# Kernel tuning notes

Hardware: AMD Instinct MI355X
Metric: run time of the kernel (lower is better)

## Reference

```python
import jax, jax.numpy as jnp
import numpy as np

BATCH = 65536
VEC = 512       # CLIP embedding dim
K = 1024        # num_cluster
GAMMA = 0.99
EPS = 1e-05


def setup_inputs() -> dict:
    key = jax.random.key(0)
    k1, k2, k3 = jax.random.split(key, 3)
    batch_vectors = jax.random.normal(k1, (BATCH, VEC), dtype=jnp.float32)
    weight = jax.random.normal(k2, (VEC, K), dtype=jnp.float32)        # codebook, stored (vec_size, num_cluster)
    cluster_size = jnp.ones((K,), dtype=jnp.float32)
    embed_avg = jax.random.normal(k3, (VEC, K), dtype=jnp.float32)
    return {
        "batch_vectors": batch_vectors,
        "weight": weight,
        "cluster_size": cluster_size,
        "embed_avg": embed_avg,
    }


def reference(batch_vectors, weight, cluster_size, embed_avg):
    """One minibatch_update step of clusteringEMA_torch.

    Returns the updated codebook `weight` of shape (vec_size, num_cluster).
    """
    gamma = GAMMA
    eps = EPS
    num_cluster = weight.shape[1]

    # nearest centroid: squared L2 distance has the same argmin as the L2 norm
    x2 = jnp.sum(batch_vectors * batch_vectors, axis=1, keepdims=True)   # (B,1)
    w2 = jnp.sum(weight * weight, axis=0)[None, :]                       # (1,K)
    dist2 = x2 + w2 - 2.0 * (batch_vectors @ weight)                     # (B,K)
    argmin = jnp.argmin(dist2, axis=-1)                                  # (B,)

    # per-cluster counts (one-hot sum), zeros replaced by 1
    counts = jnp.zeros((num_cluster,), dtype=batch_vectors.dtype).at[argmin].add(1.0)
    n_idx_choice = jnp.where(counts == 0, 1.0, counts)

    # EMA of cluster sizes
    new_cluster_size = gamma * cluster_size + (1.0 - gamma) * n_idx_choice

    # embed_sum = x^T @ onehot  == per-cluster sum of assigned vectors, (vec,K)
    embed_sum = jax.ops.segment_sum(batch_vectors, argmin, num_segments=num_cluster).T
    new_embed_avg = gamma * embed_avg + (1.0 - gamma) * embed_sum

    # Laplace-smoothed normalization
    n = jnp.sum(new_cluster_size)
    cs = (new_cluster_size + eps) / (n + num_cluster * eps) * n
    new_weight = new_embed_avg / cs[None, :]
    return new_weight
```

## Files before the change

### kernel.cpp

```cpp
#include <hip/hip_runtime.h>

typedef unsigned int uint;
typedef unsigned short ushort_t;
typedef unsigned long long u64;
typedef __attribute__((ext_vector_type(4))) float f32x4;
typedef __attribute__((ext_vector_type(8))) __bf16 bf16x8;
typedef __attribute__((ext_vector_type(8))) unsigned short us8;

#define BATCH 65536
#define VEC 512
#define K 1024
#define GAMMA 0.99f
#define EPS 1e-05f
#define SEG 64
#define MARGIN 0.75f

#define NKT (VEC / 64)
#define TG 2048

__device__ __forceinline__ ushort_t rtn(float f) {
    uint u = __float_as_uint(f);
    return (ushort_t)((u + 0x7FFFu + ((u >> 16) & 1u)) >> 16);
}

__device__ __forceinline__ void gl16(const void* g, void* l) {
    __builtin_amdgcn_global_load_lds(
        (const __attribute__((address_space(1))) unsigned int*)g,
        (__attribute__((address_space(3))) unsigned int*)l, 16, 0, 0);
}

__device__ __forceinline__ float dec_key(uint e) {
    uint b = (e & 0x80000000u) ? (e & 0x7FFFFFFFu) : ~e;
    return __uint_as_float(b);
}

#define BC8(p) __builtin_bit_cast(bf16x8, (p))

__global__ void k_pack_w(const float* __restrict__ w, us8* __restrict__ wpk,
                         float* __restrict__ wT, float* __restrict__ w2p,
                         int* __restrict__ cc ) {
    __shared__ float lds[32][257];
    const int g = blockIdx.x;
    const int gx = g >> 3, kt = g & 7;
    const int t = threadIdx.x;

    float s = 0.f;
#pragma unroll
    for (int ih = 0; ih < 2; ++ih) {
        __syncthreads();
#pragma unroll
        for (int r = 0; r < 32; ++r)
            lds[r][t] = w[(size_t)(kt * 64 + ih * 32 + r) * K + gx * 256 + t];
        __syncthreads();

#pragma unroll
        for (int r = 0; r < 32; ++r) { float f = lds[r][t]; s += f * f; }

#pragma unroll
        for (int i = 0; i < 4; ++i) {
            const int c = i * 256 + t;
            const int ct = c >> 6, lane = c & 63;
            const int cl = ct * 16 + (lane & 15);
            const int r0 = (lane >> 4) * 8;
            us8 v;
#pragma unroll
            for (int j = 0; j < 8; ++j) v[j] = rtn(lds[r0 + j][cl]);
            wpk[(size_t)g * TG + ct * 128 + ih * 64 + lane] = v;
        }

#pragma unroll
        for (int rr = 0; rr < 8; ++rr) {
            f32x4 v = {lds[rr * 4 + 0][t], lds[rr * 4 + 1][t],
                       lds[rr * 4 + 2][t], lds[rr * 4 + 3][t]};
            *(f32x4*)&wT[(size_t)(gx * 256 + t) * VEC + kt * 64 + ih * 32 + rr * 4] = v;
        }
    }
    w2p[kt * K + gx * 256 + t] = s;

    if (g < 8) cc[g * 256 + t] = 0;
    if (g == 8 && t == 0) cc[2048] = 0;
}

__global__ void k_pack_x(const float* __restrict__ x, us8* __restrict__ xpk) {
    const int blk = blockIdx.x;
    const int gy = blk >> 3, kt = blk & 7;
    const int t = threadIdx.x;
#pragma unroll
    for (int i = 0; i < 8; ++i) {
        const int g = i * 256 + t;
        const int slab = g >> 7, ksub = (g >> 6) & 1, lane = g & 63;
        const int row = gy * 256 + slab * 16 + (lane & 15);
        const int k = kt * 64 + ksub * 32 + ((lane >> 4) << 3);
        const f32x4 q0 = *(const f32x4*)&x[(size_t)row * VEC + k];
        const f32x4 q1 = *(const f32x4*)&x[(size_t)row * VEC + k + 4];
        us8 v;
#pragma unroll
        for (int j = 0; j < 4; ++j) { v[j] = rtn(q0[j]); v[4 + j] = rtn(q1[j]); }
        xpk[(size_t)blk * TG + g] = v;
    }
}

__launch_bounds__(512, 2)
__global__ void k_gemm(const us8* __restrict__ xpk, const us8* __restrict__ wpk,
                       const float* __restrict__ w2p,
                       u64* __restrict__ keysA, u64* __restrict__ keysB) {
    __shared__ us8 lds[2][2 * TG];

    const int blk = blockIdx.x;
    const int ord = blk >> 3;
    const int gy = (blk & 7) * 32 + (ord >> 2);
    const int gx = ord & 3;
    const int t = threadIdx.x;
    const int lane = t & 63;
    const int wv = t >> 6;
    const int wm = wv >> 2;
    const int wn = wv & 3;

    const us8* asrc = xpk + (size_t)gy * (NKT * TG);
    const us8* bsrc = wpk + (size_t)gx * (NKT * TG);

    auto stage = [&](int slot, int kt) {
        const us8* sa = asrc + (size_t)kt * TG;
        const us8* sb = bsrc + (size_t)kt * TG;
#pragma unroll
        for (int i = 0; i < 4; ++i) gl16(sa + i * 512 + t, &lds[slot][i * 512 + t]);
#pragma unroll
        for (int i = 0; i < 4; ++i) gl16(sb + i * 512 + t, &lds[slot][TG + i * 512 + t]);
    };

    f32x4 acc[8][4];
#pragma unroll
    for (int i = 0; i < 8; ++i)
#pragma unroll
        for (int j = 0; j < 4; ++j) acc[i][j] = (f32x4){0.f, 0.f, 0.f, 0.f};

    stage(0, 0);
    stage(1, 1);

    for (int kt = 0; kt < NKT; ++kt) {
        const int buf = kt & 1;
        if (kt >= 1 && kt + 1 < NKT) {
            stage(buf ^ 1, kt + 1);
            asm volatile("s_waitcnt vmcnt(8)" ::: "memory");
        } else if (kt == 0) {
            asm volatile("s_waitcnt vmcnt(8)" ::: "memory");
        } else {
            asm volatile("s_waitcnt vmcnt(0)" ::: "memory");
        }
        __builtin_amdgcn_s_barrier();

        const us8* A = &lds[buf][0];
        const us8* B = &lds[buf][TG];
        bf16x8 ah[8], b0, b1;

#pragma unroll
        for (int rt = 0; rt < 8; ++rt) ah[rt] = BC8(A[(wm * 8 + rt) * 128 + lane]);
        b0 = BC8(B[(wn * 4 + 0) * 128 + lane]);
        b1 = BC8(B[(wn * 4 + 1) * 128 + lane]);
        __builtin_amdgcn_s_barrier();
        asm volatile("s_waitcnt lgkmcnt(0)" ::: "memory");
        __builtin_amdgcn_sched_barrier(0);
        __builtin_amdgcn_s_setprio(1);
#pragma unroll
        for (int rt = 0; rt < 8; ++rt) {
            acc[rt][0] = __builtin_amdgcn_mfma_f32_16x16x32_bf16(ah[rt], b0, acc[rt][0], 0, 0, 0);
            acc[rt][1] = __builtin_amdgcn_mfma_f32_16x16x32_bf16(ah[rt], b1, acc[rt][1], 0, 0, 0);
        }
        __builtin_amdgcn_s_setprio(0);
        __builtin_amdgcn_s_barrier();

        b0 = BC8(B[(wn * 4 + 2) * 128 + lane]);
        b1 = BC8(B[(wn * 4 + 3) * 128 + lane]);
        __builtin_amdgcn_s_barrier();
        asm volatile("s_waitcnt lgkmcnt(0)" ::: "memory");
        __builtin_amdgcn_sched_barrier(0);
        __builtin_amdgcn_s_setprio(1);
#pragma unroll
        for (int rt = 0; rt < 8; ++rt) {
            acc[rt][2] = __builtin_amdgcn_mfma_f32_16x16x32_bf16(ah[rt], b0, acc[rt][2], 0, 0, 0);
            acc[rt][3] = __builtin_amdgcn_mfma_f32_16x16x32_bf16(ah[rt], b1, acc[rt][3], 0, 0, 0);
        }
        __builtin_amdgcn_s_setprio(0);
        __builtin_amdgcn_s_barrier();

#pragma unroll
        for (int rt = 0; rt < 8; ++rt) ah[rt] = BC8(A[(wm * 8 + rt) * 128 + 64 + lane]);
        b0 = BC8(B[(wn * 4 + 0) * 128 + 64 + lane]);
        b1 = BC8(B[(wn * 4 + 1) * 128 + 64 + lane]);
        __builtin_amdgcn_s_barrier();
        asm volatile("s_waitcnt lgkmcnt(0)" ::: "memory");
        __builtin_amdgcn_sched_barrier(0);
        __builtin_amdgcn_s_setprio(1);
#pragma unroll
        for (int rt = 0; rt < 8; ++rt) {
            acc[rt][0] = __builtin_amdgcn_mfma_f32_16x16x32_bf16(ah[rt], b0, acc[rt][0], 0, 0, 0);
            acc[rt][1] = __builtin_amdgcn_mfma_f32_16x16x32_bf16(ah[rt], b1, acc[rt][1], 0, 0, 0);
        }
        __builtin_amdgcn_s_setprio(0);
        __builtin_amdgcn_s_barrier();

        b0 = BC8(B[(wn * 4 + 2) * 128 + 64 + lane]);
        b1 = BC8(B[(wn * 4 + 3) * 128 + 64 + lane]);
        __builtin_amdgcn_s_barrier();
        asm volatile("s_waitcnt lgkmcnt(0)" ::: "memory");
        __builtin_amdgcn_sched_barrier(0);
        __builtin_amdgcn_s_setprio(1);
#pragma unroll
        for (int rt = 0; rt < 8; ++rt) {
            acc[rt][2] = __builtin_amdgcn_mfma_f32_16x16x32_bf16(ah[rt], b0, acc[rt][2], 0, 0, 0);
            acc[rt][3] = __builtin_amdgcn_mfma_f32_16x16x32_bf16(ah[rt], b1, acc[rt][3], 0, 0, 0);
        }
        __builtin_amdgcn_s_setprio(0);
        __builtin_amdgcn_s_barrier();
    }

    const int col_base = gx * 256 + wn * 64;
    float w2c[4];
#pragma unroll
    for (int ct = 0; ct < 4; ++ct) {
        const int col = col_base + ct * 16 + (lane & 15);
        float s = 0.f;
#pragma unroll
        for (int p = 0; p < 8; ++p) s += w2p[p * K + col];
        w2c[ct] = s;
    }
    const int slot = gx * 4 + wn;

#pragma unroll
    for (int rt = 0; rt < 8; ++rt) {
#pragma unroll
        for (int reg = 0; reg < 4; ++reg) {
            u64 k1 = ~0ull, k2 = ~0ull;
#pragma unroll
            for (int ct = 0; ct < 4; ++ct) {
                float dist = w2c[ct] - 2.0f * acc[rt][ct][reg];
                uint su = __float_as_uint(dist);
                su = (su & 0x80000000u) ? ~su : (su | 0x80000000u);
                const u64 key = ((u64)su << 32) | (uint)(col_base + ct * 16 + (lane & 15));
                if (key < k1) { k2 = k1; k1 = key; }
                else if (key < k2) { k2 = key; }
            }
#pragma unroll
            for (int m = 1; m < 16; m <<= 1) {
                u64 o1 = __shfl_xor((unsigned long long)k1, m);
                u64 o2 = __shfl_xor((unsigned long long)k2, m);
                u64 lo = k1 < o1 ? k1 : o1;
                u64 hi = k1 < o1 ? o1 : k1;
                u64 mn2 = k2 < o2 ? k2 : o2;
                k1 = lo;
                k2 = hi < mn2 ? hi : mn2;
            }
            if ((lane & 15) == 0) {
                const int row = gy * 256 + wm * 128 + rt * 16 + (lane >> 4) * 4 + reg;
                keysA[(size_t)slot * BATCH + row] = k1;
                keysB[(size_t)slot * BATCH + row] = k2;
            }
        }
    }
}

__global__ void k_verify(const u64* __restrict__ keysA, const u64* __restrict__ keysB,
                         int* __restrict__ am, int* __restrict__ counts,
                         u64* __restrict__ list, int* __restrict__ listcnt,
                         float* __restrict__ esum) {
    const int r = blockIdx.x * 256 + threadIdx.x;
    f32x4 z = {0.f, 0.f, 0.f, 0.f};
    ((f32x4*)esum)[r * 2] = z;
    ((f32x4*)esum)[r * 2 + 1] = z;

    u64 m1 = ~0ull, s = ~0ull;
    int i1 = 0;
#pragma unroll
    for (int i = 0; i < 16; ++i) {
        u64 a = keysA[(size_t)i * BATCH + r];
        if (a < m1) { s = m1; m1 = a; i1 = i; }
        else if (a < s) s = a;
    }
    u64 b = keysB[(size_t)i1 * BATCH + r];
    u64 m2 = s < b ? s : b;

    const float d1 = dec_key((uint)(m1 >> 32));
    const float d2 = dec_key((uint)(m2 >> 32));
    const int c1 = (int)(uint)m1 & 1023;
    const int c2 = (int)(uint)m2 & 1023;

    if (d2 - d1 > MARGIN) {
        am[r] = c1;
        atomicAdd(&counts[c1], 1);
    } else {
        int p = atomicAdd(listcnt, 1);
        list[p] = ((u64)(uint)r << 32) | ((uint)c1 << 10) | (uint)c2;
    }
}

__launch_bounds__(256)
__global__ void k_recheck(const float* __restrict__ x, const float* __restrict__ wT,
                          const float* __restrict__ w2p, const u64* __restrict__ list,
                          const int* __restrict__ listcnt, int* __restrict__ am,
                          int* __restrict__ counts) {
    const int gwid = (blockIdx.x * 256 + threadIdx.x) >> 6;
    const int lane = threadIdx.x & 63;
    const int n = *listcnt;
    for (int idx = gwid; idx < n; idx += 1024) {
        const u64 e = list[idx];
        const int r = (int)(e >> 32);
        const int c1 = (int)((e >> 10) & 1023);
        const int c2 = (int)(e & 1023);
        const f32x4 x0 = *(const f32x4*)&x[(size_t)r * VEC + lane * 8];
        const f32x4 x1 = *(const f32x4*)&x[(size_t)r * VEC + lane * 8 + 4];
        float d[2];
        const int cc2[2] = {c1, c2};
#pragma unroll
        for (int j = 0; j < 2; ++j) {
            const int c = cc2[j];
            const f32x4 w0 = *(const f32x4*)&wT[(size_t)c * VEC + lane * 8];
            const f32x4 w1 = *(const f32x4*)&wT[(size_t)c * VEC + lane * 8 + 4];
            float p = x0[0] * w0[0] + x0[1] * w0[1] + x0[2] * w0[2] + x0[3] * w0[3]
                    + x1[0] * w1[0] + x1[1] * w1[1] + x1[2] * w1[2] + x1[3] * w1[3];
#pragma unroll
            for (int m = 1; m < 64; m <<= 1) p += __shfl_xor(p, m);
            float w2 = 0.f;
#pragma unroll
            for (int q = 0; q < 8; ++q) w2 += w2p[q * K + c];
            d[j] = w2 - 2.0f * p;
        }
        const int win = (d[0] < d[1] || (d[0] == d[1] && c1 < c2)) ? c1 : c2;
        if (lane == 0) {
            am[r] = win;
            atomicAdd(&counts[win], 1);
        }
    }
}

__global__ void k_scan(const int* __restrict__ counts,
                       const float* __restrict__ cluster_size,
                       int* __restrict__ offsets, float* __restrict__ cs) {
    __shared__ int wsum[16];
    __shared__ float fw[16];
    const int t = threadIdx.x;
    const int lane = t & 63, wid = t >> 6;
    const int c = counts[t];

    int s = c;
#pragma unroll
    for (int d = 1; d < 64; d <<= 1) {
        int o = __shfl_up(s, d);
        if (lane >= d) s += o;
    }
    float ncs = GAMMA * cluster_size[t] + (1.0f - GAMMA) * ((c == 0) ? 1.0f : (float)c);
    float fs = ncs;
#pragma unroll
    for (int d = 32; d > 0; d >>= 1) fs += __shfl_xor(fs, d);

    if (lane == 63) wsum[wid] = s;
    if (lane == 0) fw[wid] = fs;
    __syncthreads();
    if (wid == 0 && lane < 16) {
        int v = wsum[lane];
#pragma unroll
        for (int d = 1; d < 16; d <<= 1) {
            int o = __shfl_up(v, d);
            if (lane >= d) v += o;
        }
        wsum[lane] = v;
    }
    __syncthreads();
    const int base = wid ? wsum[wid - 1] : 0;
    offsets[t] = base + s - c;

    float n = 0.f;
#pragma unroll
    for (int i = 0; i < 16; ++i) n += fw[i];
    cs[t] = (ncs + EPS) / (n + (float)K * EPS) * n;
}

__global__ void k_scatter(const int* __restrict__ am, const int* __restrict__ offsets,
                          int* __restrict__ cursor, int* __restrict__ sorted,
                          int* __restrict__ sortedk) {
    const int b = blockIdx.x * blockDim.x + threadIdx.x;
    const int k = am[b];
    const int pos = atomicAdd(&cursor[k], 1);
    sorted[offsets[k] + pos] = b;
    sortedk[offsets[k] + pos] = k;
}

__launch_bounds__(512)
__global__ void k_segred(const float* __restrict__ x, const int* __restrict__ sorted,
                         const int* __restrict__ sortedk, float* __restrict__ esum) {
    __shared__ int srow[SEG];
    __shared__ int skid[SEG];
    const int b = blockIdx.x;
    const int t = threadIdx.x;
    if (t < SEG) {
        srow[t] = sorted[b * SEG + t];
        skid[t] = sortedk[b * SEG + t];
    }
    __syncthreads();

    float a = 0.f;
    int cur = skid[0];
#pragma unroll 8
    for (int i = 0; i < SEG; ++i) {
        const int k = skid[i];
        if (k != cur) {
            atomicAdd(&esum[(size_t)cur * VEC + t], a);
            a = 0.f;
            cur = k;
        }
        a += x[(size_t)srow[i] * VEC + t];
    }
    atomicAdd(&esum[(size_t)cur * VEC + t], a);
}

__launch_bounds__(256)
__global__ void k_finalize(const float* __restrict__ esum, const float* __restrict__ embed_avg,
                           const float* __restrict__ cs, float* __restrict__ out) {
    __shared__ float tile[64][65];
    const int k0 = blockIdx.x * 64;
    const int v0 = blockIdx.y * 64;
    const int c = threadIdx.x & 63;
    const int r0 = threadIdx.x >> 6;
#pragma unroll
    for (int j = 0; j < 16; ++j) {
        const int r = r0 + j * 4;
        tile[r][c] = esum[(size_t)(k0 + r) * VEC + v0 + c];
    }
    __syncthreads();
    const float csk = cs[k0 + c];
#pragma unroll
    for (int j = 0; j < 16; ++j) {
        const int r = r0 + j * 4;
        const size_t o = (size_t)(v0 + r) * K + k0 + c;
        out[o] = (GAMMA * embed_avg[o] + (1.0f - GAMMA) * tile[c][r]) / csk;
    }
}

extern "C" void kernel_launch(void* const* d_in, const int* in_sizes, int n_in,
                              void* d_out, int out_size, void* d_ws, size_t ws_size,
                              hipStream_t stream) {
    const float* x            = (const float*)d_in[0];
    const float* w            = (const float*)d_in[1];
    const float* cluster_size = (const float*)d_in[2];
    const float* embed_avg    = (const float*)d_in[3];
    float* out = (float*)d_out;

    u64*   keysA   = (u64*)d_ws;
    u64*   keysB   = keysA + (size_t)16 * BATCH;
    int*   am      = (int*)(keysB + (size_t)16 * BATCH);
    u64*   list    = (u64*)(am + BATCH);
    float* w2p     = (float*)(list + BATCH);
    float* cs      = w2p + 8 * K;
    int*   cc      = (int*)(cs + K);
    int*   counts  = cc;
    int*   cursor  = cc + K;
    int*   listcnt = cc + 2 * K;
    int*   offsets = cc + 2 * K + 64;
    int*   sorted  = offsets + K;
    int*   sortedk = sorted + BATCH;
    float* esum    = (float*)(sortedk + BATCH);
    us8*   wpk     = (us8*)(esum + (size_t)K * VEC);
    float* wT      = (float*)(wpk + (size_t)32 * TG);
    us8*   xpk     = (us8*)(wT + (size_t)K * VEC);

    k_pack_w<<<32, 256, 0, stream>>>(w, wpk, wT, w2p, cc);
    k_pack_x<<<2048, 256, 0, stream>>>(x, xpk);
    k_gemm<<<1024, 512, 0, stream>>>(xpk, wpk, w2p, keysA, keysB);
    k_verify<<<BATCH / 256, 256, 0, stream>>>(keysA, keysB, am, counts, list, listcnt, esum);
    k_recheck<<<256, 256, 0, stream>>>(x, wT, w2p, list, listcnt, am, counts);
    k_scan<<<1, K, 0, stream>>>(counts, cluster_size, offsets, cs);
    k_scatter<<<BATCH / 256, 256, 0, stream>>>(am, offsets, cursor, sorted, sortedk);
    k_segred<<<BATCH / SEG, 512, 0, stream>>>(x, sorted, sortedk, esum);
    k_finalize<<<dim3(K / 64, VEC / 64), 256, 0, stream>>>(esum, embed_avg, cs, out);
}
```

Measured before the change: 413.8 us.

## Fuse pack, recheck, scan and cluster-size kernels to cut launches

Merges the weight and input packing kernels into one launch, folds the near-tie recheck into the verify kernel using a per-block shared list, and folds the prefix scan into the scatter kernel, where each block recomputes the offsets. It also moves the cluster-size normalization into finalize and restructures the GEMM inner phase to load all four B fragments at once, removing two barrier phases. Together this drops several small launches and global round trips. In exchange, work is duplicated: every scatter block redoes the scan and every finalize block redoes the size reduction, and recheck work now concentrates in whichever blocks have ties.

```diff
diff --git a/kernel.cpp b/kernel.cpp
--- a/kernel.cpp
+++ b/kernel.cpp
@@ -36,67 +36,65 @@
 
 #define BC8(p) __builtin_bit_cast(bf16x8, (p))
 
-__global__ void k_pack_w(const float* __restrict__ w, us8* __restrict__ wpk,
-                         float* __restrict__ wT, float* __restrict__ w2p,
-                         int* __restrict__ cc ) {
+__global__ void k_pack(const float* __restrict__ w, const float* __restrict__ x,
+                       us8* __restrict__ wpk, us8* __restrict__ xpk,
+                       float* __restrict__ wT, float* __restrict__ w2p,
+                       int* __restrict__ cc ) {
     __shared__ float lds[32][257];
-    const int g = blockIdx.x;
-    const int gx = g >> 3, kt = g & 7;
-    const int t = threadIdx.x;
-
-    float s = 0.f;
-#pragma unroll
-    for (int ih = 0; ih < 2; ++ih) {
-        __syncthreads();
-#pragma unroll
-        for (int r = 0; r < 32; ++r)
-            lds[r][t] = w[(size_t)(kt * 64 + ih * 32 + r) * K + gx * 256 + t];
-        __syncthreads();
-
-#pragma unroll
-        for (int r = 0; r < 32; ++r) { float f = lds[r][t]; s += f * f; }
-
-#pragma unroll
-        for (int i = 0; i < 4; ++i) {
-            const int c = i * 256 + t;
-            const int ct = c >> 6, lane = c & 63;
-            const int cl = ct * 16 + (lane & 15);
-            const int r0 = (lane >> 4) * 8;
+    const int b = blockIdx.x;
+    const int t = threadIdx.x;
+
+    if (b < 32) {
+        const int gx = b >> 3, kt = b & 7;
+        float s = 0.f;
+#pragma unroll
+        for (int ih = 0; ih < 2; ++ih) {
+            __syncthreads();
+#pragma unroll
+            for (int r = 0; r < 32; ++r)
+                lds[r][t] = w[(size_t)(kt * 64 + ih * 32 + r) * K + gx * 256 + t];
+            __syncthreads();
+
+#pragma unroll
+            for (int r = 0; r < 32; ++r) { float f = lds[r][t]; s += f * f; }
+
+#pragma unroll
+            for (int i = 0; i < 4; ++i) {
+                const int c = i * 256 + t;
+                const int ct = c >> 6, lane = c & 63;
+                const int cl = ct * 16 + (lane & 15);
+                const int r0 = (lane >> 4) * 8;
+                us8 v;
+#pragma unroll
+                for (int j = 0; j < 8; ++j) v[j] = rtn(lds[r0 + j][cl]);
+                wpk[(size_t)b * TG + ct * 128 + ih * 64 + lane] = v;
+            }
+
+#pragma unroll
+            for (int rr = 0; rr < 8; ++rr) {
+                f32x4 v = {lds[rr * 4 + 0][t], lds[rr * 4 + 1][t],
+                           lds[rr * 4 + 2][t], lds[rr * 4 + 3][t]};
+                *(f32x4*)&wT[(size_t)(gx * 256 + t) * VEC + kt * 64 + ih * 32 + rr * 4] = v;
+            }
+        }
+        w2p[kt * K + gx * 256 + t] = s;
+        if (b < 8) cc[b * 256 + t] = 0;
+    } else {
+        const int blk = b - 32;
+        const int gy = blk >> 3, kt = blk & 7;
+#pragma unroll
+        for (int i = 0; i < 8; ++i) {
+            const int g = i * 256 + t;
+            const int slab = g >> 7, ksub = (g >> 6) & 1, lane = g & 63;
+            const int row = gy * 256 + slab * 16 + (lane & 15);
+            const int k = kt * 64 + ksub * 32 + ((lane >> 4) << 3);
+            const f32x4 q0 = *(const f32x4*)&x[(size_t)row * VEC + k];
+            const f32x4 q1 = *(const f32x4*)&x[(size_t)row * VEC + k + 4];
             us8 v;
 #pragma unroll
-            for (int j = 0; j < 8; ++j) v[j] = rtn(lds[r0 + j][cl]);
-            wpk[(size_t)g * TG + ct * 128 + ih * 64 + lane] = v;
-        }
-
-#pragma unroll
-        for (int rr = 0; rr < 8; ++rr) {
-            f32x4 v = {lds[rr * 4 + 0][t], lds[rr * 4 + 1][t],
-                       lds[rr * 4 + 2][t], lds[rr * 4 + 3][t]};
-            *(f32x4*)&wT[(size_t)(gx * 256 + t) * VEC + kt * 64 + ih * 32 + rr * 4] = v;
-        }
-    }
-    w2p[kt * K + gx * 256 + t] = s;
-
-    if (g < 8) cc[g * 256 + t] = 0;
-    if (g == 8 && t == 0) cc[2048] = 0;
-}
-
-__global__ void k_pack_x(const float* __restrict__ x, us8* __restrict__ xpk) {
-    const int blk = blockIdx.x;
-    const int gy = blk >> 3, kt = blk & 7;
-    const int t = threadIdx.x;
-#pragma unroll
-    for (int i = 0; i < 8; ++i) {
-        const int g = i * 256 + t;
-        const int slab = g >> 7, ksub = (g >> 6) & 1, lane = g & 63;
-        const int row = gy * 256 + slab * 16 + (lane & 15);
-        const int k = kt * 64 + ksub * 32 + ((lane >> 4) << 3);
-        const f32x4 q0 = *(const f32x4*)&x[(size_t)row * VEC + k];
-        const f32x4 q1 = *(const f32x4*)&x[(size_t)row * VEC + k + 4];
-        us8 v;
-#pragma unroll
-        for (int j = 0; j < 4; ++j) { v[j] = rtn(q0[j]); v[4 + j] = rtn(q1[j]); }
-        xpk[(size_t)blk * TG + g] = v;
+            for (int j = 0; j < 4; ++j) { v[j] = rtn(q0[j]); v[4 + j] = rtn(q1[j]); }
+            xpk[(size_t)blk * TG + g] = v;
+        }
     }
 }
 
@@ -139,79 +137,36 @@
 
     for (int kt = 0; kt < NKT; ++kt) {
         const int buf = kt & 1;
-        if (kt >= 1 && kt + 1 < NKT) {
-            stage(buf ^ 1, kt + 1);
-            asm volatile("s_waitcnt vmcnt(8)" ::: "memory");
-        } else if (kt == 0) {
+        if (kt + 1 < NKT) {
+            if (kt >= 1) stage(buf ^ 1, kt + 1);
             asm volatile("s_waitcnt vmcnt(8)" ::: "memory");
         } else {
             asm volatile("s_waitcnt vmcnt(0)" ::: "memory");
         }
         __builtin_amdgcn_s_barrier();
 
-        const us8* A = &lds[buf][0];
-        const us8* B = &lds[buf][TG];
-        bf16x8 ah[8], b0, b1;
-
-#pragma unroll
-        for (int rt = 0; rt < 8; ++rt) ah[rt] = BC8(A[(wm * 8 + rt) * 128 + lane]);
-        b0 = BC8(B[(wn * 4 + 0) * 128 + lane]);
-        b1 = BC8(B[(wn * 4 + 1) * 128 + lane]);
-        __builtin_amdgcn_s_barrier();
-        asm volatile("s_waitcnt lgkmcnt(0)" ::: "memory");
-        __builtin_amdgcn_sched_barrier(0);
-        __builtin_amdgcn_s_setprio(1);
-#pragma unroll
-        for (int rt = 0; rt < 8; ++rt) {
-            acc[rt][0] = __builtin_amdgcn_mfma_f32_16x16x32_bf16(ah[rt], b0, acc[rt][0], 0, 0, 0);
-            acc[rt][1] = __builtin_amdgcn_mfma_f32_16x16x32_bf16(ah[rt], b1, acc[rt][1], 0, 0, 0);
-        }
-        __builtin_amdgcn_s_setprio(0);
-        __builtin_amdgcn_s_barrier();
-
-        b0 = BC8(B[(wn * 4 + 2) * 128 + lane]);
-        b1 = BC8(B[(wn * 4 + 3) * 128 + lane]);
-        __builtin_amdgcn_s_barrier();
-        asm volatile("s_waitcnt lgkmcnt(0)" ::: "memory");
-        __builtin_amdgcn_sched_barrier(0);
-        __builtin_amdgcn_s_setprio(1);
-#pragma unroll
-        for (int rt = 0; rt < 8; ++rt) {
-            acc[rt][2] = __builtin_amdgcn_mfma_f32_16x16x32_bf16(ah[rt], b0, acc[rt][2], 0, 0, 0);
-            acc[rt][3] = __builtin_amdgcn_mfma_f32_16x16x32_bf16(ah[rt], b1, acc[rt][3], 0, 0, 0);
-        }
-        __builtin_amdgcn_s_setprio(0);
-        __builtin_amdgcn_s_barrier();
-
-#pragma unroll
-        for (int rt = 0; rt < 8; ++rt) ah[rt] = BC8(A[(wm * 8 + rt) * 128 + 64 + lane]);
-        b0 = BC8(B[(wn * 4 + 0) * 128 + 64 + lane]);
-        b1 = BC8(B[(wn * 4 + 1) * 128 + 64 + lane]);
-        __builtin_amdgcn_s_barrier();
-        asm volatile("s_waitcnt lgkmcnt(0)" ::: "memory");
-        __builtin_amdgcn_sched_barrier(0);
-        __builtin_amdgcn_s_setprio(1);
-#pragma unroll
-        for (int rt = 0; rt < 8; ++rt) {
-            acc[rt][0] = __builtin_amdgcn_mfma_f32_16x16x32_bf16(ah[rt], b0, acc[rt][0], 0, 0, 0);
-            acc[rt][1] = __builtin_amdgcn_mfma_f32_16x16x32_bf16(ah[rt], b1, acc[rt][1], 0, 0, 0);
-        }
-        __builtin_amdgcn_s_setprio(0);
-        __builtin_amdgcn_s_barrier();
-
-        b0 = BC8(B[(wn * 4 + 2) * 128 + 64 + lane]);
-        b1 = BC8(B[(wn * 4 + 3) * 128 + 64 + lane]);
-        __builtin_amdgcn_s_barrier();
-        asm volatile("s_waitcnt lgkmcnt(0)" ::: "memory");
-        __builtin_amdgcn_sched_barrier(0);
-        __builtin_amdgcn_s_setprio(1);
-#pragma unroll
-        for (int rt = 0; rt < 8; ++rt) {
-            acc[rt][2] = __builtin_amdgcn_mfma_f32_16x16x32_bf16(ah[rt], b0, acc[rt][2], 0, 0, 0);
-            acc[rt][3] = __builtin_amdgcn_mfma_f32_16x16x32_bf16(ah[rt], b1, acc[rt][3], 0, 0, 0);
-        }
-        __builtin_amdgcn_s_setprio(0);
-        __builtin_amdgcn_s_barrier();
+#pragma unroll
+        for (int ph = 0; ph < 2; ++ph) {
+            const int kb = ph * 64;
+            bf16x8 ah[8], bh[4];
+#pragma unroll
+            for (int rt = 0; rt < 8; ++rt)
+                ah[rt] = BC8(lds[buf][(wm * 8 + rt) * 128 + kb + lane]);
+#pragma unroll
+            for (int ct = 0; ct < 4; ++ct)
+                bh[ct] = BC8(lds[buf][TG + (wn * 4 + ct) * 128 + kb + lane]);
+            __builtin_amdgcn_s_barrier();
+            asm volatile("s_waitcnt lgkmcnt(0)" ::: "memory");
+            __builtin_amdgcn_sched_barrier(0);
+            __builtin_amdgcn_s_setprio(1);
+#pragma unroll
+            for (int rt = 0; rt < 8; ++rt)
+#pragma unroll
+                for (int ct = 0; ct < 4; ++ct)
+                    acc[rt][ct] = __builtin_amdgcn_mfma_f32_16x16x32_bf16(ah[rt], bh[ct], acc[rt][ct], 0, 0, 0);
+            __builtin_amdgcn_s_setprio(0);
+            __builtin_amdgcn_s_barrier();
+        }
     }
 
     const int col_base = gx * 256 + wn * 64;
@@ -260,10 +215,20 @@
 }
 
 __global__ void k_verify(const u64* __restrict__ keysA, const u64* __restrict__ keysB,
+                         const float* __restrict__ x, const float* __restrict__ wT,
+                         const float* __restrict__ w2p,
                          int* __restrict__ am, int* __restrict__ counts,
-                         u64* __restrict__ list, int* __restrict__ listcnt,
                          float* __restrict__ esum) {
-    const int r = blockIdx.x * 256 + threadIdx.x;
+    __shared__ int lrow[256];
+    __shared__ int lcc[256];
+    __shared__ int lcnt;
+    const int t = threadIdx.x;
+    const int r = blockIdx.x * 256 + t;
+    const int lane = t & 63;
+
+    if (t == 0) lcnt = 0;
+    __syncthreads();
+
     f32x4 z = {0.f, 0.f, 0.f, 0.f};
     ((f32x4*)esum)[r * 2] = z;
     ((f32x4*)esum)[r * 2 + 1] = z;
@@ -288,31 +253,24 @@
         am[r] = c1;
         atomicAdd(&counts[c1], 1);
     } else {
-        int p = atomicAdd(listcnt, 1);
-        list[p] = ((u64)(uint)r << 32) | ((uint)c1 << 10) | (uint)c2;
-    }
-}
-
-__launch_bounds__(256)
-__global__ void k_recheck(const float* __restrict__ x, const float* __restrict__ wT,
-                          const float* __restrict__ w2p, const u64* __restrict__ list,
-                          const int* __restrict__ listcnt, int* __restrict__ am,
-                          int* __restrict__ counts) {
-    const int gwid = (blockIdx.x * 256 + threadIdx.x) >> 6;
-    const int lane = threadIdx.x & 63;
-    const int n = *listcnt;
-    for (int idx = gwid; idx < n; idx += 1024) {
-        const u64 e = list[idx];
-        const int r = (int)(e >> 32);
-        const int c1 = (int)((e >> 10) & 1023);
-        const int c2 = (int)(e & 1023);
-        const f32x4 x0 = *(const f32x4*)&x[(size_t)r * VEC + lane * 8];
-        const f32x4 x1 = *(const f32x4*)&x[(size_t)r * VEC + lane * 8 + 4];
+        int p = atomicAdd(&lcnt, 1);
+        lrow[p] = r;
+        lcc[p] = (c1 << 10) | c2;
+    }
+    __syncthreads();
+
+    const int n = lcnt;
+    for (int idx = t >> 6; idx < n; idx += 4) {
+        const int r2 = lrow[idx];
+        const int cc1 = lcc[idx] >> 10;
+        const int cc2 = lcc[idx] & 1023;
+        const f32x4 x0 = *(const f32x4*)&x[(size_t)r2 * VEC + lane * 8];
+        const f32x4 x1 = *(const f32x4*)&x[(size_t)r2 * VEC + lane * 8 + 4];
         float d[2];
-        const int cc2[2] = {c1, c2};
+        const int cand[2] = {cc1, cc2};
 #pragma unroll
         for (int j = 0; j < 2; ++j) {
-            const int c = cc2[j];
+            const int c = cand[j];
             const f32x4 w0 = *(const f32x4*)&wT[(size_t)c * VEC + lane * 8];
             const f32x4 w1 = *(const f32x4*)&wT[(size_t)c * VEC + lane * 8 + 4];
             float p = x0[0] * w0[0] + x0[1] * w0[1] + x0[2] * w0[2] + x0[3] * w0[3]
@@ -324,36 +282,31 @@
             for (int q = 0; q < 8; ++q) w2 += w2p[q * K + c];
             d[j] = w2 - 2.0f * p;
         }
-        const int win = (d[0] < d[1] || (d[0] == d[1] && c1 < c2)) ? c1 : c2;
+        const int win = (d[0] < d[1] || (d[0] == d[1] && cc1 < cc2)) ? cc1 : cc2;
         if (lane == 0) {
-            am[r] = win;
+            am[r2] = win;
             atomicAdd(&counts[win], 1);
         }
     }
 }
 
-__global__ void k_scan(const int* __restrict__ counts,
-                       const float* __restrict__ cluster_size,
-                       int* __restrict__ offsets, float* __restrict__ cs) {
+__launch_bounds__(1024)
+__global__ void k_scatter(const int* __restrict__ counts, const int* __restrict__ am,
+                          int* __restrict__ cursor, int* __restrict__ sorted,
+                          int* __restrict__ sortedk) {
+    __shared__ int soff[K];
     __shared__ int wsum[16];
-    __shared__ float fw[16];
     const int t = threadIdx.x;
     const int lane = t & 63, wid = t >> 6;
+
     const int c = counts[t];
-
     int s = c;
 #pragma unroll
     for (int d = 1; d < 64; d <<= 1) {
         int o = __shfl_up(s, d);
         if (lane >= d) s += o;
     }
-    float ncs = GAMMA * cluster_size[t] + (1.0f - GAMMA) * ((c == 0) ? 1.0f : (float)c);
-    float fs = ncs;
-#pragma unroll
-    for (int d = 32; d > 0; d >>= 1) fs += __shfl_xor(fs, d);
-
     if (lane == 63) wsum[wid] = s;
-    if (lane == 0) fw[wid] = fs;
     __syncthreads();
     if (wid == 0 && lane < 16) {
         int v = wsum[lane];
@@ -365,23 +318,14 @@
         wsum[lane] = v;
     }
     __syncthreads();
-    const int base = wid ? wsum[wid - 1] : 0;
-    offsets[t] = base + s - c;
-
-    float n = 0.f;
-#pragma unroll
-    for (int i = 0; i < 16; ++i) n += fw[i];
-    cs[t] = (ncs + EPS) / (n + (float)K * EPS) * n;
-}
-
-__global__ void k_scatter(const int* __restrict__ am, const int* __restrict__ offsets,
-                          int* __restrict__ cursor, int* __restrict__ sorted,
-                          int* __restrict__ sortedk) {
-    const int b = blockIdx.x * blockDim.x + threadIdx.x;
-    const int k = am[b];
+    soff[t] = (wid ? wsum[wid - 1] : 0) + s - c;
+    __syncthreads();
+
+    const int r = blockIdx.x * 1024 + t;
+    const int k = am[r];
     const int pos = atomicAdd(&cursor[k], 1);
-    sorted[offsets[k] + pos] = b;
-    sortedk[offsets[k] + pos] = k;
+    sorted[soff[k] + pos] = r;
+    sortedk[soff[k] + pos] = k;
 }
 
 __launch_bounds__(512)
@@ -414,19 +358,42 @@
 
 __launch_bounds__(256)
 __global__ void k_finalize(const float* __restrict__ esum, const float* __restrict__ embed_avg,
-                           const float* __restrict__ cs, float* __restrict__ out) {
+                           const int* __restrict__ counts,
+                           const float* __restrict__ cluster_size,
+                           float* __restrict__ out) {
     __shared__ float tile[64][65];
+    __shared__ float wred[4];
+    const int t = threadIdx.x;
     const int k0 = blockIdx.x * 64;
     const int v0 = blockIdx.y * 64;
-    const int c = threadIdx.x & 63;
-    const int r0 = threadIdx.x >> 6;
+    const int c = t & 63;
+    const int r0 = t >> 6;
+    const int lane = t & 63, wid = t >> 6;
+
+    float part = 0.f;
+#pragma unroll
+    for (int j = 0; j < 4; ++j) {
+        const int idx = t * 4 + j;
+        const int cv = counts[idx];
+        part += GAMMA * cluster_size[idx] + (1.0f - GAMMA) * ((cv == 0) ? 1.0f : (float)cv);
+    }
+#pragma unroll
+    for (int d = 32; d > 0; d >>= 1) part += __shfl_xor(part, d);
+    if (lane == 0) wred[wid] = part;
+
 #pragma unroll
     for (int j = 0; j < 16; ++j) {
         const int r = r0 + j * 4;
         tile[r][c] = esum[(size_t)(k0 + r) * VEC + v0 + c];
     }
     __syncthreads();
-    const float csk = cs[k0 + c];
+
+    const float n = (wred[0] + wred[1]) + (wred[2] + wred[3]);
+    const int kc = k0 + c;
+    const int cv = counts[kc];
+    const float ncs = GAMMA * cluster_size[kc] + (1.0f - GAMMA) * ((cv == 0) ? 1.0f : (float)cv);
+    const float csk = (ncs + EPS) / (n + (float)K * EPS) * n;
+
 #pragma unroll
     for (int j = 0; j < 16; ++j) {
         const int r = r0 + j * 4;
@@ -447,28 +414,21 @@
     u64*   keysA   = (u64*)d_ws;
     u64*   keysB   = keysA + (size_t)16 * BATCH;
     int*   am      = (int*)(keysB + (size_t)16 * BATCH);
-    u64*   list    = (u64*)(am + BATCH);
-    float* w2p     = (float*)(list + BATCH);
-    float* cs      = w2p + 8 * K;
-    int*   cc      = (int*)(cs + K);
+    float* w2p     = (float*)(am + BATCH);
+    int*   cc      = (int*)(w2p + 8 * K);
     int*   counts  = cc;
     int*   cursor  = cc + K;
-    int*   listcnt = cc + 2 * K;
-    int*   offsets = cc + 2 * K + 64;
-    int*   sorted  = offsets + K;
+    int*   sorted  = cc + 2 * K;
     int*   sortedk = sorted + BATCH;
     float* esum    = (float*)(sortedk + BATCH);
     us8*   wpk     = (us8*)(esum + (size_t)K * VEC);
     float* wT      = (float*)(wpk + (size_t)32 * TG);
     us8*   xpk     = (us8*)(wT + (size_t)K * VEC);
 
-    k_pack_w<<<32, 256, 0, stream>>>(w, wpk, wT, w2p, cc);
-    k_pack_x<<<2048, 256, 0, stream>>>(x, xpk);
+    k_pack<<<2080, 256, 0, stream>>>(w, x, wpk, xpk, wT, w2p, cc);
     k_gemm<<<1024, 512, 0, stream>>>(xpk, wpk, w2p, keysA, keysB);
-    k_verify<<<BATCH / 256, 256, 0, stream>>>(keysA, keysB, am, counts, list, listcnt, esum);
-    k_recheck<<<256, 256, 0, stream>>>(x, wT, w2p, list, listcnt, am, counts);
-    k_scan<<<1, K, 0, stream>>>(counts, cluster_size, offsets, cs);
-    k_scatter<<<BATCH / 256, 256, 0, stream>>>(am, offsets, cursor, sorted, sortedk);
+    k_verify<<<BATCH / 256, 256, 0, stream>>>(keysA, keysB, x, wT, w2p, am, counts, esum);
+    k_scatter<<<64, 1024, 0, stream>>>(counts, am, cursor, sorted, sortedk);
     k_segred<<<BATCH / SEG, 512, 0, stream>>>(x, sorted, sortedk, esum);
-    k_finalize<<<dim3(K / 64, VEC / 64), 256, 0, stream>>>(esum, embed_avg, cs, out);
-}
+    k_finalize<<<dim3(K / 64, VEC / 64), 256, 0, stream>>>(esum, embed_avg, counts, cluster_size, out);
+}
```

After: 407.2 us. Within noise of the previous version (-1.6%).
